# Performance work log

Measured on AMD Instinct MI355X. Metric: run time of the kernel, lower is better.

## Reference

```python
import jax, jax.numpy as jnp
import numpy as np

FILLER = 10.1  # filler_value from __init__
B, C, L, KEEP = 128, 16, 16384, 12288


def setup_inputs() -> dict:
    key = jax.random.key(0)
    k1, k2, k3, k4 = jax.random.split(key, 4)
    x1 = jax.random.normal(k1, (B, C, 4096), dtype=jnp.float32)
    x2 = jax.random.normal(k2, (B, C, 4096), dtype=jnp.float32)
    x3 = jax.random.normal(k3, (B, C, L), dtype=jnp.float32)
    # Scatter exactly (L - KEEP) filler entries at random positions in every row,
    # so per-row compaction yields a uniform length KEEP (required by np.stack
    # in the original module).
    u = jax.random.uniform(k4, (B, C, L))
    ranks = jnp.argsort(jnp.argsort(u, axis=-1), axis=-1)  # random permutation ranks
    fill_mask = ranks < (L - KEEP)
    x3 = jnp.where(fill_mask, jnp.float32(FILLER), x3)
    return {"x1": x1, "x2": x2, "x3": x3, "keep_len": KEEP}


def reference(x1, x2, x3, keep_len):
    # Per-row stream compaction: drop entries equal to FILLER, keep original
    # order of survivors, output fixed length keep_len.
    is_filler = x3 == jnp.float32(FILLER)          # [B, C, L] bool
    # Stable argsort moves non-filler (False=0) to the front, order-preserving.
    order = jnp.argsort(is_filler, axis=-1, stable=True)  # [B, C, L]
    compacted = jnp.take_along_axis(x3, order, axis=-1)    # [B, C, L]
    return compacted[..., :keep_len]                        # [B, C, keep_len]
```

## Files before the change

### kernel.cpp

```cpp
#include <hip/hip_runtime.h>


#define FILLER_VAL 10.1f
constexpr int L_LEN    = 16384;
constexpr int KEEP_LEN = 12288;
constexpr int BLOCK    = 256;
constexpr int NW       = BLOCK / 64;
constexpr int CHUNK    = BLOCK * 4;
constexpr int NC       = L_LEN / CHUNK;

__global__ __launch_bounds__(BLOCK) void compact_rows_kernel(
    const float* __restrict__ x3, float* __restrict__ out)
{
    const int row = blockIdx.x;
    const float* __restrict__ in = x3 + (size_t)row * L_LEN;
    float* __restrict__ o = out + (size_t)row * KEEP_LEN;

    const int tid  = threadIdx.x;
    const int lane = tid & 63;
    const int wid  = tid >> 6;
    const unsigned long long lt = (1ULL << lane) - 1ULL;

    __shared__ float stage[KEEP_LEN];
    __shared__ int wtot[NC][NW];

    float4 v[NC];
    #pragma unroll
    for (int c = 0; c < NC; ++c)
        v[c] = *reinterpret_cast<const float4*>(in + c * CHUNK + tid * 4);

    int before[NC];
    #pragma unroll
    for (int c = 0; c < NC; ++c) {
        unsigned long long m0 = __ballot(v[c].x != FILLER_VAL);
        unsigned long long m1 = __ballot(v[c].y != FILLER_VAL);
        unsigned long long m2 = __ballot(v[c].z != FILLER_VAL);
        unsigned long long m3 = __ballot(v[c].w != FILLER_VAL);
        before[c] = __popcll(m0 & lt) + __popcll(m1 & lt)
                  + __popcll(m2 & lt) + __popcll(m3 & lt);
        if (lane == 0)
            wtot[c][wid] = __popcll(m0) + __popcll(m1)
                         + __popcll(m2) + __popcll(m3);
    }
    __syncthreads();

    int run = 0;
    #pragma unroll
    for (int c = 0; c < NC; ++c) {
        int wb = run;
        #pragma unroll
        for (int w = 0; w < NW; ++w) {
            int t = wtot[c][w];
            if (w < wid) wb += t;
            run += t;
        }
        int pos = wb + before[c];
        if (v[c].x != FILLER_VAL) { if (pos < KEEP_LEN) stage[pos] = v[c].x; ++pos; }
        if (v[c].y != FILLER_VAL) { if (pos < KEEP_LEN) stage[pos] = v[c].y; ++pos; }
        if (v[c].z != FILLER_VAL) { if (pos < KEEP_LEN) stage[pos] = v[c].z; ++pos; }
        if (v[c].w != FILLER_VAL) { if (pos < KEEP_LEN) stage[pos] = v[c].w; ++pos; }
    }
    __syncthreads();

    #pragma unroll
    for (int k = 0; k < KEEP_LEN / (BLOCK * 4); ++k) {
        const int idx = (k * BLOCK + tid) * 4;
        float4 val = *reinterpret_cast<const float4*>(&stage[idx]);
        *reinterpret_cast<float4*>(&o[idx]) = val;
    }
}

extern "C" void kernel_launch(void* const* d_in, const int* in_sizes, int n_in,
                              void* d_out, int out_size, void* d_ws, size_t ws_size,
                              hipStream_t stream)
{
    const float* x3 = (const float*)d_in[2];
    float* out = (float*)d_out;

    const int rows = in_sizes[2] / L_LEN;

    compact_rows_kernel<<<rows, BLOCK, 0, stream>>>(x3, out);
}
```

Measured before the change: 256.5 us.

## Split compaction into count/scan and multi-block scatter kernels

Replaces the single per-row kernel with two passes. The first kernel counts survivors per wave segment and writes exclusive prefix bases to workspace. The second kernel launches four blocks per row, so it has more parallelism and no large shared-memory staging buffer, and each block scatters its survivors directly to global memory. In exchange, the input is read twice, there is an extra launch, and the stores become scattered scalar writes instead of coalesced float4 writes.

```diff
diff --git a/kernel.cpp b/kernel.cpp
--- a/kernel.cpp
+++ b/kernel.cpp
@@ -8,65 +8,81 @@
 constexpr int NW       = BLOCK / 64;
 constexpr int CHUNK    = BLOCK * 4;
 constexpr int NC       = L_LEN / CHUNK;
+constexpr int NSEG     = NC * NW;
 
-__global__ __launch_bounds__(BLOCK) void compact_rows_kernel(
-    const float* __restrict__ x3, float* __restrict__ out)
+__global__ __launch_bounds__(BLOCK) void count_kernel(
+    const float* __restrict__ x3, int* __restrict__ bases)
 {
     const int row = blockIdx.x;
     const float* __restrict__ in = x3 + (size_t)row * L_LEN;
+
+    const int tid  = threadIdx.x;
+    const int lane = tid & 63;
+    const int wid  = tid >> 6;
+
+    __shared__ int cnt[NSEG];
+
+    #pragma unroll
+    for (int c = 0; c < NC; ++c) {
+        float4 v = *reinterpret_cast<const float4*>(in + c * CHUNK + tid * 4);
+        unsigned long long m0 = __ballot(v.x != FILLER_VAL);
+        unsigned long long m1 = __ballot(v.y != FILLER_VAL);
+        unsigned long long m2 = __ballot(v.z != FILLER_VAL);
+        unsigned long long m3 = __ballot(v.w != FILLER_VAL);
+        if (lane == 0)
+            cnt[c * NW + wid] = __popcll(m0) + __popcll(m1)
+                              + __popcll(m2) + __popcll(m3);
+    }
+    __syncthreads();
+
+    if (tid < 64) {
+        int own = cnt[tid];
+        int x = own;
+        #pragma unroll
+        for (int d = 1; d < 64; d <<= 1) {
+            int y = __shfl_up(x, d);
+            if (lane >= d) x += y;
+        }
+        bases[row * NSEG + tid] = x - own;
+    }
+}
+
+__global__ __launch_bounds__(BLOCK) void scatter_kernel(
+    const float* __restrict__ x3, const int* __restrict__ bases,
+    float* __restrict__ out)
+{
+    const int bid = blockIdx.x;
+    const int row = bid >> 2;
+    const int q   = bid & 3;
+
+    const float* __restrict__ in = x3 + (size_t)row * L_LEN;
     float* __restrict__ o = out + (size_t)row * KEEP_LEN;
+    const int* __restrict__ rb = bases + row * NSEG;
 
     const int tid  = threadIdx.x;
     const int lane = tid & 63;
     const int wid  = tid >> 6;
     const unsigned long long lt = (1ULL << lane) - 1ULL;
 
-    __shared__ float stage[KEEP_LEN];
-    __shared__ int wtot[NC][NW];
+    #pragma unroll
+    for (int i = 0; i < NC / 4; ++i) {
+        const int c = q * (NC / 4) + i;
+        float4 v = *reinterpret_cast<const float4*>(in + c * CHUNK + tid * 4);
 
-    float4 v[NC];
-    #pragma unroll
-    for (int c = 0; c < NC; ++c)
-        v[c] = *reinterpret_cast<const float4*>(in + c * CHUNK + tid * 4);
+        unsigned long long m0 = __ballot(v.x != FILLER_VAL);
+        unsigned long long m1 = __ballot(v.y != FILLER_VAL);
+        unsigned long long m2 = __ballot(v.z != FILLER_VAL);
+        unsigned long long m3 = __ballot(v.w != FILLER_VAL);
 
-    int before[NC];
-    #pragma unroll
-    for (int c = 0; c < NC; ++c) {
-        unsigned long long m0 = __ballot(v[c].x != FILLER_VAL);
-        unsigned long long m1 = __ballot(v[c].y != FILLER_VAL);
-        unsigned long long m2 = __ballot(v[c].z != FILLER_VAL);
-        unsigned long long m3 = __ballot(v[c].w != FILLER_VAL);
-        before[c] = __popcll(m0 & lt) + __popcll(m1 & lt)
-                  + __popcll(m2 & lt) + __popcll(m3 & lt);
-        if (lane == 0)
-            wtot[c][wid] = __popcll(m0) + __popcll(m1)
-                         + __popcll(m2) + __popcll(m3);
-    }
-    __syncthreads();
+        const int before = __popcll(m0 & lt) + __popcll(m1 & lt)
+                         + __popcll(m2 & lt) + __popcll(m3 & lt);
 
-    int run = 0;
-    #pragma unroll
-    for (int c = 0; c < NC; ++c) {
-        int wb = run;
-        #pragma unroll
-        for (int w = 0; w < NW; ++w) {
-            int t = wtot[c][w];
-            if (w < wid) wb += t;
-            run += t;
-        }
-        int pos = wb + before[c];
-        if (v[c].x != FILLER_VAL) { if (pos < KEEP_LEN) stage[pos] = v[c].x; ++pos; }
-        if (v[c].y != FILLER_VAL) { if (pos < KEEP_LEN) stage[pos] = v[c].y; ++pos; }
-        if (v[c].z != FILLER_VAL) { if (pos < KEEP_LEN) stage[pos] = v[c].z; ++pos; }
-        if (v[c].w != FILLER_VAL) { if (pos < KEEP_LEN) stage[pos] = v[c].w; ++pos; }
-    }
-    __syncthreads();
+        int pos = rb[c * NW + wid] + before;
 
-    #pragma unroll
-    for (int k = 0; k < KEEP_LEN / (BLOCK * 4); ++k) {
-        const int idx = (k * BLOCK + tid) * 4;
-        float4 val = *reinterpret_cast<const float4*>(&stage[idx]);
-        *reinterpret_cast<float4*>(&o[idx]) = val;
+        if (v.x != FILLER_VAL) { if (pos < KEEP_LEN) o[pos] = v.x; ++pos; }
+        if (v.y != FILLER_VAL) { if (pos < KEEP_LEN) o[pos] = v.y; ++pos; }
+        if (v.z != FILLER_VAL) { if (pos < KEEP_LEN) o[pos] = v.z; ++pos; }
+        if (v.w != FILLER_VAL) { if (pos < KEEP_LEN) o[pos] = v.w; ++pos; }
     }
 }
 
@@ -76,8 +92,10 @@
 {
     const float* x3 = (const float*)d_in[2];
     float* out = (float*)d_out;
+    int* bases = (int*)d_ws;
 
     const int rows = in_sizes[2] / L_LEN;
 
-    compact_rows_kernel<<<rows, BLOCK, 0, stream>>>(x3, out);
+    count_kernel<<<rows, BLOCK, 0, stream>>>(x3, bases);
+    scatter_kernel<<<rows * 4, BLOCK, 0, stream>>>(x3, bases, out);
 }
```

After: 273.4 us. 6.6% more time.

## Split each row into four quarter-blocks with redundant prefix counting

Applied to the files above, without the earlier changes.

Each row is now handled by four blocks, one per 4096-element quarter, instead of one block per row. Each block re-reads the preceding quarters to count survivors and find its output offset, then compacts its own quarter into a smaller shared buffer and writes it out with scalar, unaligned stores. This gives four times as many blocks and less shared memory per block, which should improve occupancy and latency hiding. The cost is redundant global reads (on average 1.5 extra quarters per block) and non-vectorized output writes.

```diff
diff --git a/kernel.cpp b/kernel.cpp
--- a/kernel.cpp
+++ b/kernel.cpp
@@ -6,13 +6,17 @@
 constexpr int KEEP_LEN = 12288;
 constexpr int BLOCK    = 256;
 constexpr int NW       = BLOCK / 64;
-constexpr int CHUNK    = BLOCK * 4;
-constexpr int NC       = L_LEN / CHUNK;
+constexpr int QELEM    = 4096;
+constexpr int QCH      = QELEM / (BLOCK * 4);
+constexpr int NQ       = L_LEN / QELEM;
 
-__global__ __launch_bounds__(BLOCK) void compact_rows_kernel(
+__global__ __launch_bounds__(BLOCK) void compact_quarters(
     const float* __restrict__ x3, float* __restrict__ out)
 {
-    const int row = blockIdx.x;
+    const int bid = blockIdx.x;
+    const int row = bid >> 2;
+    const int q   = bid & 3;
+
     const float* __restrict__ in = x3 + (size_t)row * L_LEN;
     float* __restrict__ o = out + (size_t)row * KEEP_LEN;
 
@@ -21,17 +25,34 @@
     const int wid  = tid >> 6;
     const unsigned long long lt = (1ULL << lane) - 1ULL;
 
-    __shared__ float stage[KEEP_LEN];
-    __shared__ int wtot[NC][NW];
+    __shared__ float stage[QELEM];
+    __shared__ int   segCnt[QCH][NW];
+    __shared__ int   preW[NW];
 
-    float4 v[NC];
+    float4 v[QCH];
     #pragma unroll
-    for (int c = 0; c < NC; ++c)
-        v[c] = *reinterpret_cast<const float4*>(in + c * CHUNK + tid * 4);
+    for (int c = 0; c < QCH; ++c)
+        v[c] = *reinterpret_cast<const float4*>(
+                   in + q * QELEM + c * (BLOCK * 4) + tid * 4);
 
-    int before[NC];
+    int pre = 0;
+    for (int p = 0; p < q; ++p) {
+        #pragma unroll
+        for (int c = 0; c < QCH; ++c) {
+            float4 u = *reinterpret_cast<const float4*>(
+                           in + p * QELEM + c * (BLOCK * 4) + tid * 4);
+            unsigned long long m0 = __ballot(u.x != FILLER_VAL);
+            unsigned long long m1 = __ballot(u.y != FILLER_VAL);
+            unsigned long long m2 = __ballot(u.z != FILLER_VAL);
+            unsigned long long m3 = __ballot(u.w != FILLER_VAL);
+            pre += __popcll(m0) + __popcll(m1) + __popcll(m2) + __popcll(m3);
+        }
+    }
+    if (lane == 0) preW[wid] = pre;
+
+    int before[QCH];
     #pragma unroll
-    for (int c = 0; c < NC; ++c) {
+    for (int c = 0; c < QCH; ++c) {
         unsigned long long m0 = __ballot(v[c].x != FILLER_VAL);
         unsigned long long m1 = __ballot(v[c].y != FILLER_VAL);
         unsigned long long m2 = __ballot(v[c].z != FILLER_VAL);
@@ -39,35 +60,44 @@
         before[c] = __popcll(m0 & lt) + __popcll(m1 & lt)
                   + __popcll(m2 & lt) + __popcll(m3 & lt);
         if (lane == 0)
-            wtot[c][wid] = __popcll(m0) + __popcll(m1)
-                         + __popcll(m2) + __popcll(m3);
+            segCnt[c][wid] = __popcll(m0) + __popcll(m1)
+                           + __popcll(m2) + __popcll(m3);
     }
     __syncthreads();
 
+    int base = 0;
+    #pragma unroll
+    for (int w = 0; w < NW; ++w) base += preW[w];
+
     int run = 0;
+    int myseg[QCH];
     #pragma unroll
-    for (int c = 0; c < NC; ++c) {
+    for (int c = 0; c < QCH; ++c) {
         int wb = run;
         #pragma unroll
         for (int w = 0; w < NW; ++w) {
-            int t = wtot[c][w];
+            int t = segCnt[c][w];
             if (w < wid) wb += t;
             run += t;
         }
-        int pos = wb + before[c];
-        if (v[c].x != FILLER_VAL) { if (pos < KEEP_LEN) stage[pos] = v[c].x; ++pos; }
-        if (v[c].y != FILLER_VAL) { if (pos < KEEP_LEN) stage[pos] = v[c].y; ++pos; }
-        if (v[c].z != FILLER_VAL) { if (pos < KEEP_LEN) stage[pos] = v[c].z; ++pos; }
-        if (v[c].w != FILLER_VAL) { if (pos < KEEP_LEN) stage[pos] = v[c].w; ++pos; }
+        myseg[c] = wb;
+    }
+    const int cnt_total = run;
+
+    #pragma unroll
+    for (int c = 0; c < QCH; ++c) {
+        int pos = myseg[c] + before[c];
+        if (v[c].x != FILLER_VAL) { if (pos < QELEM) stage[pos] = v[c].x; ++pos; }
+        if (v[c].y != FILLER_VAL) { if (pos < QELEM) stage[pos] = v[c].y; ++pos; }
+        if (v[c].z != FILLER_VAL) { if (pos < QELEM) stage[pos] = v[c].z; ++pos; }
+        if (v[c].w != FILLER_VAL) { if (pos < QELEM) stage[pos] = v[c].w; ++pos; }
     }
     __syncthreads();
 
-    #pragma unroll
-    for (int k = 0; k < KEEP_LEN / (BLOCK * 4); ++k) {
-        const int idx = (k * BLOCK + tid) * 4;
-        float4 val = *reinterpret_cast<const float4*>(&stage[idx]);
-        *reinterpret_cast<float4*>(&o[idx]) = val;
-    }
+    int gend = base + cnt_total;
+    if (gend > KEEP_LEN) gend = KEEP_LEN;
+    for (int i = base + tid; i < gend; i += BLOCK)
+        o[i] = stage[i - base];
 }
 
 extern "C" void kernel_launch(void* const* d_in, const int* in_sizes, int n_in,
@@ -79,5 +109,5 @@
 
     const int rows = in_sizes[2] / L_LEN;
 
-    compact_rows_kernel<<<rows, BLOCK, 0, stream>>>(x3, out);
+    compact_quarters<<<rows * NQ, BLOCK, 0, stream>>>(x3, out);
 }
```

New measurement: 269.6 us. 1.05x slower.
